# Optimization experiments

Hardware: AMD Instinct MI355X
Metric: run time of the kernel (lower is better)

## Reference

```python
import jax, jax.numpy as jnp
import numpy as np


def setup_inputs() -> dict:
    key = jax.random.key(0)
    B, D = 4096, 1024
    ks = jax.random.split(key, 4)
    return {
        "text_embed": jax.random.normal(ks[0], (B, D), dtype=jnp.float32),
        "image_embed": jax.random.normal(ks[1], (B, D), dtype=jnp.float32),
        "audio_embed": jax.random.normal(ks[2], (B, D), dtype=jnp.float32),
        "depth_embed": jax.random.normal(ks[3], (B, D), dtype=jnp.float32),
        # CLIP-style temperature already exponentiated (~100 at convergence)
        "logit_scale": jnp.ones((1,), dtype=jnp.float32) * 100.0,
    }


def _contrastive_pair(feat1, feat2_all, logit_scale):
    # logits[i,j] = scale * <feat1_i, feat2_j>; labels = arange(B) -> diagonal
    logits = logit_scale * (feat1 @ feat2_all.T)          # [B, B]
    logp = jax.nn.log_softmax(logits, axis=-1)
    return -jnp.mean(jnp.diagonal(logp))


def reference(text_embed, image_embed, audio_embed, depth_embed, logit_scale):
    s = logit_scale[0]
    total = jnp.float32(0.0)
    for m_emb in (audio_embed, depth_embed):
        # modality <-> text
        l_m2t = _contrastive_pair(m_emb, text_embed, s)
        l_t2m = _contrastive_pair(text_embed, m_emb, s)
        total = total + (l_m2t + l_t2m) / 2
        # modality <-> image
        l_m2i = _contrastive_pair(m_emb, image_embed, s)
        l_i2m = _contrastive_pair(image_embed, m_emb, s)
        total = total + (l_m2i + l_i2m) / 2
    # text <-> image
    l_t2i = _contrastive_pair(text_embed, image_embed, s)
    l_i2t = _contrastive_pair(image_embed, text_embed, s)
    total = total + (l_t2i + l_i2t) / 2
    return total
```

## Files before the change

### kernel.cpp

```cpp
#include <hip/hip_runtime.h>
#include <hip/hip_bf16.h>

#define BDIM 4096
#define DDIM 1024
#define NPAIRS 5
#define TW 16
#define KT 16
#define LDS_MAT 16384

typedef __attribute__((ext_vector_type(8))) short short8;
typedef __attribute__((ext_vector_type(4))) float floatx4;

__device__ __forceinline__ void gload16(const void* g, void* l) {
    __builtin_amdgcn_global_load_lds((const __attribute__((address_space(1))) void*)g,
                                     (__attribute__((address_space(3))) void*)l, 16, 0, 0);
}

__device__ __forceinline__ unsigned short f2bf(float f) {
    unsigned u = __float_as_uint(f);
    u = (u + 0x7FFFu + ((u >> 16) & 1u)) >> 16;
    return (unsigned short)u;
}

__global__ void cast_kernel(const float* __restrict__ t, const float* __restrict__ im,
                            const float* __restrict__ au, const float* __restrict__ de,
                            short* __restrict__ out) {
    const float* src;
    switch (blockIdx.y) {
        case 0: src = t; break;
        case 1: src = im; break;
        case 2: src = au; break;
        default: src = de; break;
    }
    short* dst = out + (size_t)blockIdx.y * (BDIM * DDIM);
    int idx = (blockIdx.x * 256 + threadIdx.x) * 8;
    float4 f0 = *(const float4*)(src + idx);
    float4 f1 = *(const float4*)(src + idx + 4);
    short8 r;
    r[0] = (short)f2bf(f0.x); r[1] = (short)f2bf(f0.y);
    r[2] = (short)f2bf(f0.z); r[3] = (short)f2bf(f0.w);
    r[4] = (short)f2bf(f1.x); r[5] = (short)f2bf(f1.y);
    r[6] = (short)f2bf(f1.z); r[7] = (short)f2bf(f1.w);
    *(short8*)(dst + idx) = r;
}

__device__ __forceinline__ void stage_mat(const short* __restrict__ gsrc, short* ldst,
                                          int w, int l, int k0) {
    const int lr = l >> 3;
    const int lc = ((l & 7) ^ lr) * 8;
#pragma unroll
    for (int i = 0; i < 4; ++i) {
        int s = w * 4 + i;
        gload16(gsrc + (s * 8 + lr) * DDIM + k0 + lc, (char*)ldst + s * 1024);
    }
}

__device__ __forceinline__ short8 ldsfrag(const short* buf, int row, int kofShorts) {
    int slot = kofShorts >> 3;
    return *(const short8*)((const char*)buf + row * 128 + ((slot ^ (row & 7)) << 4));
}

__device__ __forceinline__ float vsel4(floatx4 v, int j) {
    return (j == 0) ? v[0] : (j == 1) ? v[1] : (j == 2) ? v[2] : v[3];
}

__launch_bounds__(512, 1)
__global__ void gemm_lse_kernel(const short* __restrict__ mats, const float* __restrict__ scale_p,
                                float* __restrict__ rowpart, float* __restrict__ colpart,
                                float* __restrict__ diag) {
    extern __shared__ char smem[];
    short* As = (short*)smem;
    short* Bs = (short*)(smem + 65536);
    float* rowLse = (float*)(smem + 131072);
    float* colLse = rowLse + 4 * 256;

    const int tid = threadIdx.x;
    const int w = tid >> 6, l = tid & 63;
    const int wr = w >> 2, wc = w & 3;

    const int orig = blockIdx.x;
    const int swz = (orig & 7) * 160 + (orig >> 3);
    const int p = swz >> 8;
    const int t = swz & 255;
    const int tileRow = t & 15, tileCol = t >> 4;

    int ai, bi;
    switch (p) {
        case 0: ai = 2; bi = 0; break;
        case 1: ai = 2; bi = 1; break;
        case 2: ai = 3; bi = 0; break;
        case 3: ai = 3; bi = 1; break;
        default: ai = 0; bi = 1; break;
    }
    const short* Aop = mats + (size_t)ai * (BDIM * DDIM) + tileRow * 256 * DDIM;
    const short* Bop = mats + (size_t)bi * (BDIM * DDIM) + tileCol * 256 * DDIM;
    const float s = scale_p[0];

    floatx4 acc[8][4];
#pragma unroll
    for (int m = 0; m < 8; ++m)
#pragma unroll
        for (int n = 0; n < 4; ++n) acc[m][n] = (floatx4)(0.f);

    const int fr = l & 15, hi = l >> 4;
    const int arow = wr * 128 + fr;
    const int brow = wc * 64 + fr;

    stage_mat(Aop, As, w, l, 0);
    stage_mat(Bop, Bs, w, l, 0);
    __syncthreads();

    for (int kt = 0; kt < KT; ++kt) {
        const short* a_buf = As + (kt & 1) * LDS_MAT;
        const short* b_buf = Bs + (kt & 1) * LDS_MAT;
        short* a_nxt = As + ((kt + 1) & 1) * LDS_MAT;
        short* b_nxt = Bs + ((kt + 1) & 1) * LDS_MAT;

        if (kt < KT - 1) {
            const int k0n = (kt + 1) * 64;
            stage_mat(Aop, a_nxt, w, l, k0n);
            stage_mat(Bop, b_nxt, w, l, k0n);
        }

        short8 bfr[2][4];
#pragma unroll
        for (int kk = 0; kk < 2; ++kk)
#pragma unroll
            for (int n = 0; n < 4; ++n)
                bfr[kk][n] = ldsfrag(b_buf, brow + n * 16, kk * 32 + hi * 8);

#pragma unroll
        for (int m = 0; m < 8; ++m) {
            short8 afr0 = ldsfrag(a_buf, arow + m * 16, hi * 8);
            short8 afr1 = ldsfrag(a_buf, arow + m * 16, 32 + hi * 8);
            __builtin_amdgcn_s_setprio(1);
#pragma unroll
            for (int n = 0; n < 4; ++n)
                acc[m][n] = __builtin_amdgcn_mfma_f32_16x16x32_bf16(afr0, bfr[0][n], acc[m][n], 0, 0, 0);
#pragma unroll
            for (int n = 0; n < 4; ++n)
                acc[m][n] = __builtin_amdgcn_mfma_f32_16x16x32_bf16(afr1, bfr[1][n], acc[m][n], 0, 0, 0);
            __builtin_amdgcn_s_setprio(0);
        }
        __syncthreads();
    }

#pragma unroll
    for (int m = 0; m < 8; ++m)
#pragma unroll
        for (int n = 0; n < 4; ++n)
#pragma unroll
            for (int j = 0; j < 4; ++j) acc[m][n][j] *= s;


#pragma unroll
    for (int m = 0; m < 8; ++m) {
#pragma unroll
        for (int j = 0; j < 4; ++j) {
            float mx = -3.0e38f;
#pragma unroll
            for (int n = 0; n < 4; ++n) mx = fmaxf(mx, acc[m][n][j]);
#pragma unroll
            for (int off = 1; off < 16; off <<= 1) mx = fmaxf(mx, __shfl_xor(mx, off));
            float sm = 0.f;
#pragma unroll
            for (int n = 0; n < 4; ++n) sm += __expf(acc[m][n][j] - mx);
#pragma unroll
            for (int off = 1; off < 16; off <<= 1) sm += __shfl_xor(sm, off);
            if (fr == 0)
                rowLse[wc * 256 + wr * 128 + m * 16 + hi * 4 + j] = mx + __logf(sm);
        }
    }

#pragma unroll
    for (int n = 0; n < 4; ++n) {
        float mx = -3.0e38f;
#pragma unroll
        for (int m = 0; m < 8; ++m)
#pragma unroll
            for (int j = 0; j < 4; ++j) mx = fmaxf(mx, acc[m][n][j]);
        mx = fmaxf(mx, __shfl_xor(mx, 16));
        mx = fmaxf(mx, __shfl_xor(mx, 32));
        float sm = 0.f;
#pragma unroll
        for (int m = 0; m < 8; ++m)
#pragma unroll
            for (int j = 0; j < 4; ++j) sm += __expf(acc[m][n][j] - mx);
        sm += __shfl_xor(sm, 16);
        sm += __shfl_xor(sm, 32);
        if (hi == 0)
            colLse[wr * 256 + wc * 64 + n * 16 + fr] = mx + __logf(sm);
    }

    if (tileRow == tileCol && (wc >> 1) == wr) {
        if (hi == (fr >> 2)) {
            const int j = fr & 3;
            float* dst = diag + p * BDIM + tileRow * 256 + wc * 64 + fr;
            if ((wc & 1) == 0) {
                dst[0]  = vsel4(acc[0][0], j);
                dst[16] = vsel4(acc[1][1], j);
                dst[32] = vsel4(acc[2][2], j);
                dst[48] = vsel4(acc[3][3], j);
            } else {
                dst[0]  = vsel4(acc[4][0], j);
                dst[16] = vsel4(acc[5][1], j);
                dst[32] = vsel4(acc[6][2], j);
                dst[48] = vsel4(acc[7][3], j);
            }
        }
    }

    __syncthreads();

    if (tid < 256) {
        float v0 = rowLse[tid], v1 = rowLse[256 + tid], v2 = rowLse[512 + tid], v3 = rowLse[768 + tid];
        float mm = fmaxf(fmaxf(v0, v1), fmaxf(v2, v3));
        float r = mm + __logf(__expf(v0 - mm) + __expf(v1 - mm) + __expf(v2 - mm) + __expf(v3 - mm));
        rowpart[((size_t)p * BDIM + tileRow * 256 + tid) * TW + tileCol] = r;
    } else {
        int c = tid - 256;
        float v0 = colLse[c], v1 = colLse[256 + c];
        float mm = fmaxf(v0, v1);
        float r = mm + __logf(__expf(v0 - mm) + __expf(v1 - mm));
        colpart[((size_t)p * BDIM + tileCol * 256 + c) * TW + tileRow] = r;
    }
}

__global__ void reduce_kernel(const float* __restrict__ rowpart, const float* __restrict__ colpart,
                              const float* __restrict__ diag, float* __restrict__ partials) {
    int p = blockIdx.y;
    int i = blockIdx.x * 256 + threadIdx.x;
    size_t gi = (size_t)p * BDIM + i;

    const float* rp = rowpart + gi * TW;
    float mx = -3.0e38f;
#pragma unroll
    for (int t = 0; t < TW; ++t) mx = fmaxf(mx, rp[t]);
    float sm = 0.f;
#pragma unroll
    for (int t = 0; t < TW; ++t) sm += __expf(rp[t] - mx);
    float rl = mx + __logf(sm);

    const float* cp = colpart + gi * TW;
    mx = -3.0e38f;
#pragma unroll
    for (int t = 0; t < TW; ++t) mx = fmaxf(mx, cp[t]);
    sm = 0.f;
#pragma unroll
    for (int t = 0; t < TW; ++t) sm += __expf(cp[t] - mx);
    float cl = mx + __logf(sm);

    float contrib = rl + cl - 2.f * diag[gi];

    __shared__ float red[256];
    red[threadIdx.x] = contrib;
    __syncthreads();
    for (int s2 = 128; s2 > 0; s2 >>= 1) {
        if (threadIdx.x < (unsigned)s2) red[threadIdx.x] += red[threadIdx.x + s2];
        __syncthreads();
    }
    if (threadIdx.x == 0) partials[p * 16 + blockIdx.x] = red[0];
}

__global__ void final_kernel(const float* __restrict__ partials, float* __restrict__ out) {
    __shared__ float red[128];
    int t = threadIdx.x;
    red[t] = (t < NPAIRS * 16) ? partials[t] : 0.f;
    __syncthreads();
    for (int s2 = 64; s2 > 0; s2 >>= 1) {
        if (t < s2) red[t] += red[t + s2];
        __syncthreads();
    }
    if (t == 0) out[0] = red[0] * (1.f / (2.f * BDIM));
}

extern "C" void kernel_launch(void* const* d_in, const int* in_sizes, int n_in,
                              void* d_out, int out_size, void* d_ws, size_t ws_size,
                              hipStream_t stream) {
    const float* text  = (const float*)d_in[0];
    const float* image = (const float*)d_in[1];
    const float* audio = (const float*)d_in[2];
    const float* depth = (const float*)d_in[3];
    const float* scale = (const float*)d_in[4];
    float* out = (float*)d_out;

    char* ws = (char*)d_ws;
    short* mats = (short*)ws;
    size_t off = (size_t)4 * BDIM * DDIM * 2;
    float* rowpart = (float*)(ws + off); off += (size_t)NPAIRS * BDIM * TW * 4;
    float* colpart = (float*)(ws + off); off += (size_t)NPAIRS * BDIM * TW * 4;
    float* diag    = (float*)(ws + off); off += (size_t)NPAIRS * BDIM * 4;
    float* partials= (float*)(ws + off); off += NPAIRS * 16 * 4;

    const int smem_bytes = 131072 + 4 * 256 * 4 + 2 * 256 * 4;
    hipFuncSetAttribute((const void*)gemm_lse_kernel,
                        hipFuncAttributeMaxDynamicSharedMemorySize, smem_bytes);

    cast_kernel<<<dim3(2048, 4), 256, 0, stream>>>(text, image, audio, depth, mats);
    gemm_lse_kernel<<<dim3(1280), 512, smem_bytes, stream>>>(mats, scale, rowpart, colpart, diag);
    reduce_kernel<<<dim3(16, NPAIRS), 256, 0, stream>>>(rowpart, colpart, diag, partials);
    final_kernel<<<1, 128, 0, stream>>>(partials, out);
}
```

Measured before the change: 231.1 us.

## Restructure GEMM mainloop into 4-stage K=32 pipeline with vmcnt-based waits

Replaces the double-buffered K=64 tile loop with a four-buffer ring of K=32 half-tiles. Loads are prefetched three stages ahead, with partial s_waitcnt vmcnt waits and raw barriers instead of full __syncthreads. Global-to-LDS staging is interleaved between the two MFMA groups of each step. The goal is to hide global load latency and lower per-iteration barrier stalls, at the cost of twice as many barriers and tighter correctness dependence on the hand-counted vmcnt values.

Measured after the change: 236.7 us. +2.4%, slower.

```diff
diff --git a/kernel.cpp b/kernel.cpp
--- a/kernel.cpp
+++ b/kernel.cpp
@@ -5,8 +5,8 @@
 #define DDIM 1024
 #define NPAIRS 5
 #define TW 16
-#define KT 16
-#define LDS_MAT 16384
+#define NH 32
+#define HBUF 8192
 
 typedef __attribute__((ext_vector_type(8))) short short8;
 typedef __attribute__((ext_vector_type(4))) float floatx4;
@@ -44,24 +44,58 @@
     *(short8*)(dst + idx) = r;
 }
 
-__device__ __forceinline__ void stage_mat(const short* __restrict__ gsrc, short* ldst,
-                                          int w, int l, int k0) {
-    const int lr = l >> 3;
-    const int lc = ((l & 7) ^ lr) * 8;
-#pragma unroll
-    for (int i = 0; i < 4; ++i) {
-        int s = w * 4 + i;
-        gload16(gsrc + (s * 8 + lr) * DDIM + k0 + lc, (char*)ldst + s * 1024);
-    }
-}
-
-__device__ __forceinline__ short8 ldsfrag(const short* buf, int row, int kofShorts) {
+__device__ __forceinline__ void stage_half(const short* __restrict__ gsrc, short* ldst,
+                                           int w, int l, int k0) {
+    const int r0 = w * 16 + (l >> 2);
+    const int kof = ((l & 3) ^ ((l >> 2) & 3)) * 8;
+#pragma unroll
+    for (int i = 0; i < 2; ++i) {
+        int row = i * 128 + r0;
+        gload16(gsrc + (size_t)row * DDIM + k0 + kof,
+                (char*)ldst + i * 8192 + w * 1024 + l * 16);
+    }
+}
+
+__device__ __forceinline__ short8 ldsfrag32(const short* buf, int row, int kofShorts) {
     int slot = kofShorts >> 3;
-    return *(const short8*)((const char*)buf + row * 128 + ((slot ^ (row & 7)) << 4));
+    return *(const short8*)((const char*)buf + row * 64 + ((slot ^ (row & 3)) << 4));
 }
 
 __device__ __forceinline__ float vsel4(floatx4 v, int j) {
     return (j == 0) ? v[0] : (j == 1) ? v[1] : (j == 2) ? v[2] : v[3];
+}
+
+__device__ __forceinline__ void khalf(floatx4 (&acc)[8][4],
+                                      const short* a_buf, const short* b_buf,
+                                      short* a_nxt, short* b_nxt,
+                                      const short* __restrict__ Aop,
+                                      const short* __restrict__ Bop,
+                                      int w, int l, int arow, int brow, int hi,
+                                      int k0n, bool doStage) {
+    short8 bfr[4];
+#pragma unroll
+    for (int n = 0; n < 4; ++n) bfr[n] = ldsfrag32(b_buf, brow + n * 16, hi * 8);
+    short8 afr[4];
+#pragma unroll
+    for (int m = 0; m < 4; ++m) afr[m] = ldsfrag32(a_buf, arow + m * 16, hi * 8);
+    if (doStage) stage_half(Aop, a_nxt, w, l, k0n);
+    __builtin_amdgcn_s_setprio(1);
+#pragma unroll
+    for (int m = 0; m < 4; ++m)
+#pragma unroll
+        for (int n = 0; n < 4; ++n)
+            acc[m][n] = __builtin_amdgcn_mfma_f32_16x16x32_bf16(afr[m], bfr[n], acc[m][n], 0, 0, 0);
+    __builtin_amdgcn_s_setprio(0);
+#pragma unroll
+    for (int m = 0; m < 4; ++m) afr[m] = ldsfrag32(a_buf, arow + (m + 4) * 16, hi * 8);
+    if (doStage) stage_half(Bop, b_nxt, w, l, k0n);
+    __builtin_amdgcn_s_setprio(1);
+#pragma unroll
+    for (int m = 0; m < 4; ++m)
+#pragma unroll
+        for (int n = 0; n < 4; ++n)
+            acc[m + 4][n] = __builtin_amdgcn_mfma_f32_16x16x32_bf16(afr[m], bfr[n], acc[m + 4][n], 0, 0, 0);
+    __builtin_amdgcn_s_setprio(0);
 }
 
 __launch_bounds__(512, 1)
@@ -94,7 +128,6 @@
     }
     const short* Aop = mats + (size_t)ai * (BDIM * DDIM) + tileRow * 256 * DDIM;
     const short* Bop = mats + (size_t)bi * (BDIM * DDIM) + tileCol * 256 * DDIM;
-    const float s = scale_p[0];
 
     floatx4 acc[8][4];
 #pragma unroll
@@ -106,45 +139,39 @@
     const int arow = wr * 128 + fr;
     const int brow = wc * 64 + fr;
 
-    stage_mat(Aop, As, w, l, 0);
-    stage_mat(Bop, Bs, w, l, 0);
-    __syncthreads();
-
-    for (int kt = 0; kt < KT; ++kt) {
-        const short* a_buf = As + (kt & 1) * LDS_MAT;
-        const short* b_buf = Bs + (kt & 1) * LDS_MAT;
-        short* a_nxt = As + ((kt + 1) & 1) * LDS_MAT;
-        short* b_nxt = Bs + ((kt + 1) & 1) * LDS_MAT;
-
-        if (kt < KT - 1) {
-            const int k0n = (kt + 1) * 64;
-            stage_mat(Aop, a_nxt, w, l, k0n);
-            stage_mat(Bop, b_nxt, w, l, k0n);
-        }
-
-        short8 bfr[2][4];
-#pragma unroll
-        for (int kk = 0; kk < 2; ++kk)
-#pragma unroll
-            for (int n = 0; n < 4; ++n)
-                bfr[kk][n] = ldsfrag(b_buf, brow + n * 16, kk * 32 + hi * 8);
-
-#pragma unroll
-        for (int m = 0; m < 8; ++m) {
-            short8 afr0 = ldsfrag(a_buf, arow + m * 16, hi * 8);
-            short8 afr1 = ldsfrag(a_buf, arow + m * 16, 32 + hi * 8);
-            __builtin_amdgcn_s_setprio(1);
-#pragma unroll
-            for (int n = 0; n < 4; ++n)
-                acc[m][n] = __builtin_amdgcn_mfma_f32_16x16x32_bf16(afr0, bfr[0][n], acc[m][n], 0, 0, 0);
-#pragma unroll
-            for (int n = 0; n < 4; ++n)
-                acc[m][n] = __builtin_amdgcn_mfma_f32_16x16x32_bf16(afr1, bfr[1][n], acc[m][n], 0, 0, 0);
-            __builtin_amdgcn_s_setprio(0);
-        }
-        __syncthreads();
-    }
-
+    stage_half(Aop, As + 0 * HBUF, w, l, 0);
+    stage_half(Bop, Bs + 0 * HBUF, w, l, 0);
+    stage_half(Aop, As + 1 * HBUF, w, l, 32);
+    stage_half(Bop, Bs + 1 * HBUF, w, l, 32);
+    stage_half(Aop, As + 2 * HBUF, w, l, 64);
+    stage_half(Bop, Bs + 2 * HBUF, w, l, 64);
+    asm volatile("s_waitcnt vmcnt(8)" ::: "memory");
+    __builtin_amdgcn_s_barrier();
+
+#pragma unroll 4
+    for (int h = 0; h < 28; ++h) {
+        const int hb = h & 3, nb = (h + 3) & 3;
+        khalf(acc, As + hb * HBUF, Bs + hb * HBUF, As + nb * HBUF, Bs + nb * HBUF,
+              Aop, Bop, w, l, arow, brow, hi, (h + 3) * 32, true);
+        asm volatile("s_waitcnt vmcnt(8)" ::: "memory");
+        __builtin_amdgcn_s_barrier();
+    }
+    khalf(acc, As + 0 * HBUF, Bs + 0 * HBUF, As + 3 * HBUF, Bs + 3 * HBUF,
+          Aop, Bop, w, l, arow, brow, hi, 31 * 32, true);
+    asm volatile("s_waitcnt vmcnt(8)" ::: "memory");
+    __builtin_amdgcn_s_barrier();
+    khalf(acc, As + 1 * HBUF, Bs + 1 * HBUF, As + 0 * HBUF, Bs + 0 * HBUF,
+          Aop, Bop, w, l, arow, brow, hi, 0, false);
+    asm volatile("s_waitcnt vmcnt(4)" ::: "memory");
+    __builtin_amdgcn_s_barrier();
+    khalf(acc, As + 2 * HBUF, Bs + 2 * HBUF, As + 0 * HBUF, Bs + 0 * HBUF,
+          Aop, Bop, w, l, arow, brow, hi, 0, false);
+    asm volatile("s_waitcnt vmcnt(0)" ::: "memory");
+    __builtin_amdgcn_s_barrier();
+    khalf(acc, As + 3 * HBUF, Bs + 3 * HBUF, As + 0 * HBUF, Bs + 0 * HBUF,
+          Aop, Bop, w, l, arow, brow, hi, 0, false);
+
+    const float s = scale_p[0];
 #pragma unroll
     for (int m = 0; m < 8; ++m)
 #pragma unroll
```

## Split K tiles into half-regions with fine-grained staged prefetch and explicit waitcnt scheduling

Applied to the files above, without the earlier changes.

Replaces the per-K-tile double-buffered staging with a four-region LDS layout of 32-wide K halves. Global-to-LDS loads for later regions are issued partway through the current tile and guarded by explicit vmcnt/lgkmcnt waits and sched barriers. MFMAs are grouped in 8x2 bursts with a new swizzle for 64-byte rows. The goal is to overlap global loads with MFMA more tightly and replace the full __syncthreads with finer barriers. The hand-tuned wait counts are fragile, and a wrong count could cause races.

Measured after the change: 234.2 us. Within noise of the previous version (+1.3%).

```diff
diff --git a/kernel.cpp b/kernel.cpp
--- a/kernel.cpp
+++ b/kernel.cpp
@@ -6,7 +6,7 @@
 #define NPAIRS 5
 #define TW 16
 #define KT 16
-#define LDS_MAT 16384
+#define RSH 8192
 
 typedef __attribute__((ext_vector_type(8))) short short8;
 typedef __attribute__((ext_vector_type(4))) float floatx4;
@@ -44,25 +44,61 @@
     *(short8*)(dst + idx) = r;
 }
 
-__device__ __forceinline__ void stage_mat(const short* __restrict__ gsrc, short* ldst,
-                                          int w, int l, int k0) {
-    const int lr = l >> 3;
-    const int lc = ((l & 7) ^ lr) * 8;
-#pragma unroll
-    for (int i = 0; i < 4; ++i) {
-        int s = w * 4 + i;
-        gload16(gsrc + (s * 8 + lr) * DDIM + k0 + lc, (char*)ldst + s * 1024);
-    }
-}
-
-__device__ __forceinline__ short8 ldsfrag(const short* buf, int row, int kofShorts) {
-    int slot = kofShorts >> 3;
-    return *(const short8*)((const char*)buf + row * 128 + ((slot ^ (row & 7)) << 4));
+__device__ __forceinline__ void stage_region(const short* __restrict__ gsrc, short* reg,
+                                             int w, int l, int k0) {
+    const int r0 = w * 16 + (l >> 2);
+    const int kof = ((l & 3) ^ ((l >> 3) & 3)) * 8;
+#pragma unroll
+    for (int i = 0; i < 2; ++i) {
+        gload16(gsrc + (size_t)(i * 128 + r0) * DDIM + k0 + kof,
+                (char*)reg + i * 8192 + w * 1024 + l * 16);
+    }
+}
+
+__device__ __forceinline__ short8 ldsfrag32(const short* reg, int row, int hi) {
+    return *(const short8*)((const char*)reg + row * 64 + ((hi ^ ((row >> 1) & 3)) << 4));
 }
 
 __device__ __forceinline__ float vsel4(floatx4 v, int j) {
     return (j == 0) ? v[0] : (j == 1) ? v[1] : (j == 2) ? v[2] : v[3];
 }
+
+#define SBAR()  do { __builtin_amdgcn_sched_barrier(0); __builtin_amdgcn_s_barrier(); } while (0)
+#define WAITVL(vm) do { asm volatile("s_waitcnt vmcnt(" #vm ") lgkmcnt(0)" ::: "memory"); \
+                        __builtin_amdgcn_sched_barrier(0); } while (0)
+#define WAITL() do { asm volatile("s_waitcnt lgkmcnt(0)" ::: "memory"); \
+                     __builtin_amdgcn_sched_barrier(0); } while (0)
+
+#define MFMA8x2(NB) do { __builtin_amdgcn_s_setprio(1); \
+    _Pragma("unroll") for (int m_ = 0; m_ < 8; ++m_) { \
+        acc[m_][NB]     = __builtin_amdgcn_mfma_f32_16x16x32_bf16(afr[m_], b0, acc[m_][NB], 0, 0, 0); \
+        acc[m_][NB + 1] = __builtin_amdgcn_mfma_f32_16x16x32_bf16(afr[m_], b1, acc[m_][NB + 1], 0, 0, 0); } \
+    __builtin_amdgcn_s_setprio(0); } while (0)
+
+#define TILE_BODY(T, VM0, VM2, S0, S1, S2, S3) do { \
+    const short* Ar0 = As + (((T) & 1) * 2 + 0) * RSH; \
+    const short* Br0 = Bs + (((T) & 1) * 2 + 0) * RSH; \
+    const short* Ar1 = As + (((T) & 1) * 2 + 1) * RSH; \
+    const short* Br1 = Bs + (((T) & 1) * 2 + 1) * RSH; \
+     \
+    _Pragma("unroll") for (int m_ = 0; m_ < 8; ++m_) afr[m_] = ldsfrag32(Ar0, arow + m_ * 16, hi); \
+    b0 = ldsfrag32(Br0, brow + 0, hi); b1 = ldsfrag32(Br0, brow + 16, hi); \
+    if (S0) stage_region(Bop, Bs + ((((T) + 1) & 1) * 2 + 1) * RSH, w, l, ((T) + 1) * 64 + 32); \
+    SBAR(); WAITVL(VM0); MFMA8x2(0); SBAR(); \
+     \
+    b0 = ldsfrag32(Br0, brow + 32, hi); b1 = ldsfrag32(Br0, brow + 48, hi); \
+    if (S1) stage_region(Aop, As + (((T) & 1) * 2 + 0) * RSH, w, l, ((T) + 2) * 64); \
+    SBAR(); WAITL(); MFMA8x2(2); SBAR(); \
+     \
+    _Pragma("unroll") for (int m_ = 0; m_ < 8; ++m_) afr[m_] = ldsfrag32(Ar1, arow + m_ * 16, hi); \
+    b0 = ldsfrag32(Br1, brow + 0, hi); b1 = ldsfrag32(Br1, brow + 16, hi); \
+    if (S2) stage_region(Bop, Bs + (((T) & 1) * 2 + 0) * RSH, w, l, ((T) + 2) * 64); \
+    SBAR(); WAITVL(VM2); MFMA8x2(0); SBAR(); \
+     \
+    b0 = ldsfrag32(Br1, brow + 32, hi); b1 = ldsfrag32(Br1, brow + 48, hi); \
+    if (S3) stage_region(Aop, As + (((T) & 1) * 2 + 1) * RSH, w, l, ((T) + 2) * 64 + 32); \
+    SBAR(); WAITL(); MFMA8x2(2); SBAR(); \
+} while (0)
 
 __launch_bounds__(512, 1)
 __global__ void gemm_lse_kernel(const short* __restrict__ mats, const float* __restrict__ scale_p,
@@ -94,7 +130,6 @@
     }
     const short* Aop = mats + (size_t)ai * (BDIM * DDIM) + tileRow * 256 * DDIM;
     const short* Bop = mats + (size_t)bi * (BDIM * DDIM) + tileCol * 256 * DDIM;
-    const float s = scale_p[0];
 
     floatx4 acc[8][4];
 #pragma unroll
@@ -106,45 +141,24 @@
     const int arow = wr * 128 + fr;
     const int brow = wc * 64 + fr;
 
-    stage_mat(Aop, As, w, l, 0);
-    stage_mat(Bop, Bs, w, l, 0);
-    __syncthreads();
-
-    for (int kt = 0; kt < KT; ++kt) {
-        const short* a_buf = As + (kt & 1) * LDS_MAT;
-        const short* b_buf = Bs + (kt & 1) * LDS_MAT;
-        short* a_nxt = As + ((kt + 1) & 1) * LDS_MAT;
-        short* b_nxt = Bs + ((kt + 1) & 1) * LDS_MAT;
-
-        if (kt < KT - 1) {
-            const int k0n = (kt + 1) * 64;
-            stage_mat(Aop, a_nxt, w, l, k0n);
-            stage_mat(Bop, b_nxt, w, l, k0n);
-        }
-
-        short8 bfr[2][4];
-#pragma unroll
-        for (int kk = 0; kk < 2; ++kk)
-#pragma unroll
-            for (int n = 0; n < 4; ++n)
-                bfr[kk][n] = ldsfrag(b_buf, brow + n * 16, kk * 32 + hi * 8);
-
-#pragma unroll
-        for (int m = 0; m < 8; ++m) {
-            short8 afr0 = ldsfrag(a_buf, arow + m * 16, hi * 8);
-            short8 afr1 = ldsfrag(a_buf, arow + m * 16, 32 + hi * 8);
-            __builtin_amdgcn_s_setprio(1);
-#pragma unroll
-            for (int n = 0; n < 4; ++n)
-                acc[m][n] = __builtin_amdgcn_mfma_f32_16x16x32_bf16(afr0, bfr[0][n], acc[m][n], 0, 0, 0);
-#pragma unroll
-            for (int n = 0; n < 4; ++n)
-                acc[m][n] = __builtin_amdgcn_mfma_f32_16x16x32_bf16(afr1, bfr[1][n], acc[m][n], 0, 0, 0);
-            __builtin_amdgcn_s_setprio(0);
-        }
-        __syncthreads();
-    }
-
+    short8 afr[8], b0, b1;
+
+    stage_region(Aop, As + 0 * RSH, w, l, 0);
+    stage_region(Bop, Bs + 0 * RSH, w, l, 0);
+    stage_region(Aop, As + 1 * RSH, w, l, 32);
+    stage_region(Bop, Bs + 1 * RSH, w, l, 32);
+    stage_region(Aop, As + 2 * RSH, w, l, 64);
+    stage_region(Bop, Bs + 2 * RSH, w, l, 64);
+    stage_region(Aop, As + 3 * RSH, w, l, 96);
+    asm volatile("s_waitcnt vmcnt(10)" ::: "memory");
+    __builtin_amdgcn_s_barrier();
+
+#pragma unroll 2
+    for (int kt = 0; kt < 14; ++kt) TILE_BODY(kt, 8, 8, 1, 1, 1, 1);
+    TILE_BODY(14, 8, 4, 1, 0, 0, 0);
+    TILE_BODY(15, 0, 0, 0, 0, 0, 0);
+
+    const float s = scale_p[0];
 #pragma unroll
     for (int m = 0; m < 8; ++m)
 #pragma unroll
```

## Restructure GEMM main loop into fine-grained ping-pong phases with half-tile staging

Applied to the files above, without the earlier changes.

Replaces the simple double-buffered K loop with an explicitly scheduled 8-phase pipeline. Each phase overlaps LDS fragment reads, MFMA work on previously loaded fragments and half-tile global-to-LDS loads. It uses sched_barrier, s_barrier and manual waitcnt to control interleaving. The goal is to hide LDS and global latency behind MFMA issue. In exchange it adds register pressure and fragile hand-tuned wait counts that could cause races if any count is wrong.

Result: slower. 414.5 us (+79.3%).

```diff
diff --git a/kernel.cpp b/kernel.cpp
--- a/kernel.cpp
+++ b/kernel.cpp
@@ -5,8 +5,6 @@
 #define DDIM 1024
 #define NPAIRS 5
 #define TW 16
-#define KT 16
-#define LDS_MAT 16384
 
 typedef __attribute__((ext_vector_type(8))) short short8;
 typedef __attribute__((ext_vector_type(4))) float floatx4;
@@ -44,14 +42,14 @@
     *(short8*)(dst + idx) = r;
 }
 
-__device__ __forceinline__ void stage_mat(const short* __restrict__ gsrc, short* ldst,
-                                          int w, int l, int k0) {
+__device__ __forceinline__ void stage_half(const short* __restrict__ gsrc, void* lbase,
+                                           int w, int l, int k0, int ih) {
     const int lr = l >> 3;
     const int lc = ((l & 7) ^ lr) * 8;
 #pragma unroll
-    for (int i = 0; i < 4; ++i) {
-        int s = w * 4 + i;
-        gload16(gsrc + (s * 8 + lr) * DDIM + k0 + lc, (char*)ldst + s * 1024);
+    for (int j = 0; j < 2; ++j) {
+        int s = w * 4 + ih * 2 + j;
+        gload16(gsrc + (size_t)(s * 8 + lr) * DDIM + k0 + lc, (char*)lbase + s * 1024);
     }
 }
 
@@ -63,14 +61,49 @@
 __device__ __forceinline__ float vsel4(floatx4 v, int j) {
     return (j == 0) ? v[0] : (j == 1) ? v[1] : (j == 2) ? v[2] : v[3];
 }
+
+#define RD_A(DST, BUF, MH) \
+    _Pragma("unroll") for (int kk_ = 0; kk_ < 2; ++kk_) \
+    _Pragma("unroll") for (int m_ = 0; m_ < 4; ++m_) \
+        DST[kk_ * 4 + m_] = ldsfrag(BUF, arow + ((MH) * 4 + m_) * 16, kk_ * 32 + hi * 8);
+
+#define RD_B(DST, BUF, NH) \
+    _Pragma("unroll") for (int kk_ = 0; kk_ < 2; ++kk_) \
+    _Pragma("unroll") for (int n_ = 0; n_ < 2; ++n_) \
+        DST[kk_ * 2 + n_] = ldsfrag(BUF, brow + ((NH) * 2 + n_) * 16, kk_ * 32 + hi * 8);
+
+#define MF(ASET, BSET, MH, NB) \
+    _Pragma("unroll") for (int kk_ = 0; kk_ < 2; ++kk_) \
+    _Pragma("unroll") for (int m_ = 0; m_ < 4; ++m_) \
+    _Pragma("unroll") for (int n_ = 0; n_ < 2; ++n_) \
+        acc[(MH) * 4 + m_][(NB) + n_] = __builtin_amdgcn_mfma_f32_16x16x32_bf16( \
+            ASET[kk_ * 4 + m_], BSET[kk_ * 2 + n_], acc[(MH) * 4 + m_][(NB) + n_], 0, 0, 0);
+
+#define WV(n) asm volatile("s_waitcnt vmcnt(" #n ")" ::: "memory");
+
+#define PHASE(RDBLK, NL, MFBLK, STBLK, WVBLK) \
+    RDBLK \
+    __builtin_amdgcn_sched_barrier(0); \
+    __builtin_amdgcn_s_barrier(); \
+    asm volatile("s_waitcnt lgkmcnt(" #NL ")" ::: "memory"); \
+    __builtin_amdgcn_sched_barrier(0); \
+    __builtin_amdgcn_s_setprio(1); \
+    MFBLK \
+    __builtin_amdgcn_s_setprio(0); \
+    STBLK \
+    WVBLK \
+    __builtin_amdgcn_sched_barrier(0); \
+    __builtin_amdgcn_s_barrier();
 
 __launch_bounds__(512, 1)
 __global__ void gemm_lse_kernel(const short* __restrict__ mats, const float* __restrict__ scale_p,
                                 float* __restrict__ rowpart, float* __restrict__ colpart,
                                 float* __restrict__ diag) {
     extern __shared__ char smem[];
-    short* As = (short*)smem;
-    short* Bs = (short*)(smem + 65536);
+    short* Abuf0 = (short*)smem;
+    short* Abuf1 = Abuf0 + 16384;
+    short* Bbuf0 = (short*)(smem + 65536);
+    short* Bbuf1 = Bbuf0 + 16384;
     float* rowLse = (float*)(smem + 131072);
     float* colLse = rowLse + 4 * 256;
 
@@ -94,7 +127,6 @@
     }
     const short* Aop = mats + (size_t)ai * (BDIM * DDIM) + tileRow * 256 * DDIM;
     const short* Bop = mats + (size_t)bi * (BDIM * DDIM) + tileCol * 256 * DDIM;
-    const float s = scale_p[0];
 
     floatx4 acc[8][4];
 #pragma unroll
@@ -106,45 +138,44 @@
     const int arow = wr * 128 + fr;
     const int brow = wc * 64 + fr;
 
-    stage_mat(Aop, As, w, l, 0);
-    stage_mat(Bop, Bs, w, l, 0);
-    __syncthreads();
-
-    for (int kt = 0; kt < KT; ++kt) {
-        const short* a_buf = As + (kt & 1) * LDS_MAT;
-        const short* b_buf = Bs + (kt & 1) * LDS_MAT;
-        short* a_nxt = As + ((kt + 1) & 1) * LDS_MAT;
-        short* b_nxt = Bs + ((kt + 1) & 1) * LDS_MAT;
-
-        if (kt < KT - 1) {
-            const int k0n = (kt + 1) * 64;
-            stage_mat(Aop, a_nxt, w, l, k0n);
-            stage_mat(Bop, b_nxt, w, l, k0n);
-        }
-
-        short8 bfr[2][4];
-#pragma unroll
-        for (int kk = 0; kk < 2; ++kk)
-#pragma unroll
-            for (int n = 0; n < 4; ++n)
-                bfr[kk][n] = ldsfrag(b_buf, brow + n * 16, kk * 32 + hi * 8);
-
-#pragma unroll
-        for (int m = 0; m < 8; ++m) {
-            short8 afr0 = ldsfrag(a_buf, arow + m * 16, hi * 8);
-            short8 afr1 = ldsfrag(a_buf, arow + m * 16, 32 + hi * 8);
-            __builtin_amdgcn_s_setprio(1);
-#pragma unroll
-            for (int n = 0; n < 4; ++n)
-                acc[m][n] = __builtin_amdgcn_mfma_f32_16x16x32_bf16(afr0, bfr[0][n], acc[m][n], 0, 0, 0);
-#pragma unroll
-            for (int n = 0; n < 4; ++n)
-                acc[m][n] = __builtin_amdgcn_mfma_f32_16x16x32_bf16(afr1, bfr[1][n], acc[m][n], 0, 0, 0);
-            __builtin_amdgcn_s_setprio(0);
-        }
-        __syncthreads();
-    }
-
+    short8 aL[8], aH[8], bb0[4], bb1[4];
+
+    stage_half(Aop, Abuf0, w, l, 0, 0);  stage_half(Aop, Abuf0, w, l, 0, 1);
+    stage_half(Bop, Bbuf0, w, l, 0, 0);  stage_half(Bop, Bbuf0, w, l, 0, 1);
+    stage_half(Bop, Bbuf1, w, l, 64, 0); stage_half(Bop, Bbuf1, w, l, 64, 1);
+    WV(4)
+    __builtin_amdgcn_sched_barrier(0);
+    __builtin_amdgcn_s_barrier();
+    RD_A(aL, Abuf0, 0)
+    RD_B(bb0, Bbuf0, 0)
+
+#pragma unroll 1
+    for (int tp = 0; tp < 7; ++tp) {
+        const int kA1 = (2 * tp + 1) * 64;
+        const int kE2 = (2 * tp + 2) * 64;
+        const int kO3 = (2 * tp + 3) * 64;
+        PHASE(RD_A(aH, Abuf0, 1), 8, MF(aL, bb0, 0, 0), stage_half(Aop, Abuf1, w, l, kA1, 0);, )
+        PHASE(RD_B(bb1, Bbuf0, 1), 4, MF(aH, bb0, 1, 0), stage_half(Aop, Abuf1, w, l, kA1, 1);, WV(4))
+        PHASE(RD_B(bb0, Bbuf1, 0), 4, MF(aH, bb1, 1, 2), stage_half(Bop, Bbuf0, w, l, kE2, 0);, WV(2))
+        PHASE(RD_A(aH, Abuf1, 1), 8, MF(aL, bb1, 0, 2), stage_half(Bop, Bbuf0, w, l, kE2, 1);, )
+        PHASE(RD_A(aL, Abuf1, 0), 8, MF(aH, bb0, 1, 0), stage_half(Aop, Abuf0, w, l, kE2, 0);, )
+        PHASE(RD_B(bb1, Bbuf1, 1), 4, MF(aL, bb0, 0, 0), stage_half(Aop, Abuf0, w, l, kE2, 1);, WV(4))
+        PHASE(RD_B(bb0, Bbuf0, 0), 4, MF(aL, bb1, 0, 2), stage_half(Bop, Bbuf1, w, l, kO3, 0);, WV(2))
+        PHASE(RD_A(aL, Abuf0, 0), 8, MF(aH, bb1, 1, 2), stage_half(Bop, Bbuf1, w, l, kO3, 1);, )
+    }
+    {
+        const int kA1 = 15 * 64;
+        PHASE(RD_A(aH, Abuf0, 1), 8, MF(aL, bb0, 0, 0), stage_half(Aop, Abuf1, w, l, kA1, 0);, )
+        PHASE(RD_B(bb1, Bbuf0, 1), 4, MF(aH, bb0, 1, 0), stage_half(Aop, Abuf1, w, l, kA1, 1);, WV(4))
+        PHASE(RD_B(bb0, Bbuf1, 0), 4, MF(aH, bb1, 1, 2), , WV(0))
+        PHASE(RD_A(aH, Abuf1, 1), 8, MF(aL, bb1, 0, 2), , )
+        PHASE(RD_A(aL, Abuf1, 0), 8, MF(aH, bb0, 1, 0), , )
+        PHASE(RD_B(bb1, Bbuf1, 1), 4, MF(aL, bb0, 0, 0), , )
+        PHASE(, 0, MF(aL, bb1, 0, 2), , )
+        PHASE(, 0, MF(aH, bb1, 1, 2), , )
+    }
+
+    const float s = scale_p[0];
 #pragma unroll
     for (int m = 0; m < 8; ++m)
 #pragma unroll
```
